# Optimization experiments

Hardware: AMD Instinct MI355X
Metric: run time of the kernel (lower is better)

The kernel has to match this reference:

```python
import jax, jax.numpy as jnp
import numpy as np

B = 262144
IN, H = 2, 50


def setup_inputs() -> dict:
    key = jax.random.key(0)
    ks = jax.random.split(key, 12)
    k = 1.0 / np.sqrt(H)
    u = lambda kk, shape: jax.random.uniform(kk, shape, jnp.float32, -k, k)
    return {
        "s": jax.random.normal(ks[0], (B, IN), jnp.float32),
        "h": jax.random.normal(ks[1], (B, H), jnp.float32),
        "w_ih": u(ks[2], (3 * H, IN)),
        "w_hh": u(ks[3], (3 * H, H)),
        "b_ih": u(ks[4], (3 * H,)),
        "b_hh": u(ks[5], (3 * H,)),
        "actor_w": u(ks[6], (2, H)),
        "actor_b": u(ks[7], (2,)),
        "critic_w": u(ks[8], (1, H)),
        "critic_b": u(ks[9], (1,)),
    }


def reference(s, h, w_ih, w_hh, b_ih, b_hh, actor_w, actor_b, critic_w, critic_b):
    # PyTorch GRUCell gate math (gate order: reset, update, new)
    gi = s @ w_ih.T + b_ih          # [B, 3H]
    gh = h @ w_hh.T + b_hh          # [B, 3H]
    i_r, i_z, i_n = jnp.split(gi, 3, axis=1)
    h_r, h_z, h_n = jnp.split(gh, 3, axis=1)
    r = jax.nn.sigmoid(i_r + h_r)
    z = jax.nn.sigmoid(i_z + h_z)
    n = jnp.tanh(i_n + r * h_n)
    h_new = (1.0 - z) * n + z * h   # [B, H]
    c = h_new @ critic_w.T + critic_b            # [B, 1]
    pi = jax.nn.softmax(h_new @ actor_w.T + actor_b, axis=1)  # [B, 2]
    return h_new, c, pi
```

## Files before the change

### kernel.cpp

```cpp
#include <hip/hip_runtime.h>
#include <hip/hip_bf16.h>


#define BDIM 1024

typedef __bf16 bf16x8 __attribute__((ext_vector_type(8)));
typedef float f32x4 __attribute__((ext_vector_type(4)));
typedef unsigned __attribute__((may_alias)) u32a;
typedef unsigned short __attribute__((may_alias)) u16a;

__device__ __forceinline__ float bf2f(unsigned short u) {
    union { unsigned u; float f; } x; x.u = ((unsigned)u) << 16; return x.f;
}
__device__ __forceinline__ unsigned short f2bf(float f) {
    union { float f; unsigned u; } x; x.f = f;
    unsigned r = x.u + 0x7fffu + ((x.u >> 16) & 1u);
    return (unsigned short)(r >> 16);
}
__device__ __forceinline__ unsigned packbf(float a, float b) {
    union { __hip_bfloat162 h; unsigned u; } c;
    c.h = __float22bfloat162_rn(make_float2(a, b));
    return c.u;
}
__device__ __forceinline__ bf16x8 ldsfrag(const unsigned short* p) {
    bf16x8 v; __builtin_memcpy(&v, p, 16); return v;
}

template <int CTRL>
__device__ __forceinline__ float dpp_add(float v) {
    int s = __builtin_bit_cast(int, v);
    int r = __builtin_amdgcn_update_dpp(s, s, CTRL, 0xf, 0xf, false);
    return v + __builtin_bit_cast(float, r);
}
__device__ __forceinline__ float row16_sum(float v) {
    v = dpp_add<0x128>(v);
    v = dpp_add<0x124>(v);
    v = dpp_add<0x122>(v);
    v = dpp_add<0x121>(v);
    return v;
}

#define PROCESS_TILE(BT, PF)                                                 \
  do {                                                                       \
    const int rowbase = (BT) * 256;                                          \
    asm volatile("" ::: "memory");                                           \
    _Pragma("unroll")                                                        \
    for (int j = 0; j < 6; ++j) {                                            \
        int d = lane + j * 64;                                               \
        int r = d / 25, dk = d - r * 25;                                     \
        xlds32[(R + r) * 36 + dk] = packbf(PF[j].x, PF[j].y);                \
    }                                                                        \
    if (lane < 16)                                                           \
        xlds32[(R + 15) * 36 + 9 + lane] = packbf(PF[6].x, PF[6].y);         \
    else if (lane < 32)                                                      \
        xlds32[(R + lane - 16) * 36 + 25] = packbf(PF[6].x, PF[6].y);        \
    asm volatile("" ::: "memory");                                           \
    float2 srow[4];                                                          \
    _Pragma("unroll")                                                        \
    for (int reg = 0; reg < 4; ++reg)                                        \
        srow[reg] = s2[rowbase + R + quad * 4 + reg];                        \
    const unsigned short* arow = &xlds[(R + c16) * 72 + quad * 8];           \
    bf16x8 a0 = ldsfrag(arow);                                 \
    bf16x8 a1 = ldsfrag(arow + 32);                            \
    float* ob = out + (long long)rowbase * 50;      \
    float hn_r[4][4];                                                        \
    _Pragma("unroll")                                                        \
    for (int t = 0; t < 4; ++t) {                                            \
        f32x4 ar = {0.f,0.f,0.f,0.f}, az = ar, an = ar;                      \
        const int tb = (t * 128 + lane) * 8;   \
        bf16x8 br0 = ldsfrag(&wlds[tb]);                                     \
        bf16x8 br1 = ldsfrag(&wlds[tb + 512]);                               \
        bf16x8 bz0 = ldsfrag(&wlds[tb + 4096]);                              \
        bf16x8 bz1 = ldsfrag(&wlds[tb + 4608]);                              \
        bf16x8 bn0 = ldsfrag(&wlds[tb + 8192]);                              \
        bf16x8 bn1 = ldsfrag(&wlds[tb + 8704]);                              \
        ar = __builtin_amdgcn_mfma_f32_16x16x32_bf16(a0, br0, ar, 0, 0, 0);  \
        ar = __builtin_amdgcn_mfma_f32_16x16x32_bf16(a1, br1, ar, 0, 0, 0);  \
        az = __builtin_amdgcn_mfma_f32_16x16x32_bf16(a0, bz0, az, 0, 0, 0);  \
        az = __builtin_amdgcn_mfma_f32_16x16x32_bf16(a1, bz1, az, 0, 0, 0);  \
        an = __builtin_amdgcn_mfma_f32_16x16x32_bf16(a0, bn0, an, 0, 0, 0);  \
        an = __builtin_amdgcn_mfma_f32_16x16x32_bf16(a1, bn1, an, 0, 0, 0);  \
        int j = t * 16 + c16;                                                \
        _Pragma("unroll")                                                    \
        for (int reg = 0; reg < 4; ++reg) {                                  \
            int lr = R + quad * 4 + reg;          \
            float inn = fmaf(srow[reg].y, wi1[t],                            \
                        fmaf(srow[reg].x, wi0[t], bi[t]));                   \
            float rg = __builtin_amdgcn_rcpf(1.f + __expf(-ar[reg]));        \
            float zg = __builtin_amdgcn_rcpf(1.f + __expf(-az[reg]));        \
            float x = inn + rg * an[reg];                                    \
            float e2 = __expf(2.f * x);    \
            float ng = 1.f - 2.f * __builtin_amdgcn_rcpf(e2 + 1.f);          \
            float hv = bf2f(((const u16a*)xlds)[lr * 72 + j]);               \
            float hnew = fmaf(zg, hv - ng, ng);                              \
            hn_r[reg][t] = (j < 50) ? hnew : 0.f;                            \
            if (j < 50) ob[lr * 50 + j] = hnew;                              \
        }                                                                    \
    }                                                                        \
    float sum0[4], sum1[4], sumc[4];                                         \
    _Pragma("unroll")                                                        \
    for (int reg = 0; reg < 4; ++reg) {                                      \
        float p0 = 0.f, p1 = 0.f, pc = 0.f;                                  \
        _Pragma("unroll")                                                    \
        for (int t = 0; t < 4; ++t) {                                        \
            p0 = fmaf(hn_r[reg][t], aw0[t], p0);                             \
            p1 = fmaf(hn_r[reg][t], aw1[t], p1);                             \
            pc = fmaf(hn_r[reg][t], awc[t], pc);                             \
        }                                                                    \
        sum0[reg] = row16_sum(p0);                                           \
        sum1[reg] = row16_sum(p1);                                           \
        sumc[reg] = row16_sum(pc);                                           \
    }                                                                        \
    if (c16 < 4) {                  \
        float A0 = (c16 == 0) ? sum0[0] : (c16 == 1) ? sum0[1]               \
                 : (c16 == 2) ? sum0[2] : sum0[3];                           \
        float A1 = (c16 == 0) ? sum1[0] : (c16 == 1) ? sum1[1]               \
                 : (c16 == 2) ? sum1[2] : sum1[3];                           \
        float C  = (c16 == 0) ? sumc[0] : (c16 == 1) ? sumc[1]               \
                 : (c16 == 2) ? sumc[2] : sumc[3];                           \
        int gr = rowbase + R + quad * 4 + c16;                               \
        oc[gr] = C + cb;                                                     \
        A0 += ab0; A1 += ab1;                                                \
        float m = fmaxf(A0, A1);                                             \
        float e0 = __expf(A0 - m), e1 = __expf(A1 - m);                      \
        float inv = 1.f / (e0 + e1);                                         \
        float2 pv; pv.x = e0 * inv; pv.y = e1 * inv;                         \
        opi[gr] = pv;                                                        \
    }                                                                        \
  } while (0)

__global__ __launch_bounds__(BDIM, 4) void gru_fused(
    const float* __restrict__ s,
    const float* __restrict__ h,
    const float* __restrict__ w_ih,
    const float* __restrict__ w_hh,
    const float* __restrict__ b_ih,
    const float* __restrict__ b_hh,
    const float* __restrict__ actor_w,
    const float* __restrict__ actor_b,
    const float* __restrict__ critic_w,
    const float* __restrict__ critic_b,
    float* __restrict__ out,
    int Btot, int nTiles)
{
    __shared__ __align__(16) unsigned short xlds[256 * 72];
    __shared__ __align__(16) unsigned short wlds[1536 * 8];

    const int tid  = threadIdx.x;
    const int wave = tid >> 6;
    const int lane = tid & 63;
    const int c16  = lane & 15;
    const int quad = lane >> 4;
    const int R    = wave * 16;

    u32a* xlds32 = (u32a*)xlds;
    const float2* h2 = (const float2*)h;
    const float2* s2 = (const float2*)s;

    const int bt0 = blockIdx.x;
    const int bt1 = bt0 + (int)gridDim.x;
    const bool has2 = (bt1 < nTiles);
    float2 pf0[7], pf1[7];
    {
        long long hb = (long long)(bt0 * 256 + R) * 25;
        #pragma unroll
        for (int j = 0; j < 6; ++j) pf0[j] = h2[hb + lane + j * 64];
        if (lane < 16)      pf0[6] = h2[hb + 384 + lane];
        else if (lane < 32) pf0[6] = s2[bt0 * 256 + R + lane - 16];
    }
    {
        const int pb = has2 ? bt1 : bt0;
        long long hb = (long long)(pb * 256 + R) * 25;
        #pragma unroll
        for (int j = 0; j < 6; ++j) pf1[j] = h2[hb + lane + j * 64];
        if (lane < 16)      pf1[6] = h2[hb + 384 + lane];
        else if (lane < 32) pf1[6] = s2[pb * 256 + R + lane - 16];
    }

    for (int i = tid; i < 256 * 36; i += BDIM)
        xlds32[i] = ((i % 36) == 26) ? 0x00003f80u : 0u;

    for (int e = tid; e < 1536; e += BDIM) {
        int ln = e & 63;
        int ks = (e >> 6) & 1;
        int t  = (e >> 7) & 3;
        int g  = e >> 9;
        int n  = t * 16 + (ln & 15);
        int kbase = ks * 32 + (ln >> 4) * 8;
        unsigned short vals[8];
        if (n < 50) {
            int r = g * 50 + n;
            #pragma unroll
            for (int i = 0; i < 8; ++i) {
                int k = kbase + i;
                float v = 0.f;
                if (k < 50)       v = w_hh[r * 50 + k];
                else if (k == 50) v = (g < 2) ? w_ih[r * 2 + 0] : 0.f;
                else if (k == 51) v = (g < 2) ? w_ih[r * 2 + 1] : 0.f;
                else if (k == 52) {
                    v = b_hh[r];
                    if (g < 2) v += b_ih[r];
                }
                vals[i] = f2bf(v);
            }
        } else {
            #pragma unroll
            for (int i = 0; i < 8; ++i) vals[i] = 0;
        }
        #pragma unroll
        for (int i = 0; i < 8; ++i) wlds[e * 8 + i] = vals[i];
    }

    float wi0[4], wi1[4], bi[4], aw0[4], aw1[4], awc[4];
    #pragma unroll
    for (int t = 0; t < 4; ++t) {
        int j = t * 16 + c16;
        bool ok = (j < 50);
        wi0[t] = ok ? w_ih[(100 + j) * 2 + 0] : 0.f;
        wi1[t] = ok ? w_ih[(100 + j) * 2 + 1] : 0.f;
        bi[t]  = ok ? b_ih[100 + j]           : 0.f;
        aw0[t] = ok ? actor_w[j]              : 0.f;
        aw1[t] = ok ? actor_w[50 + j]         : 0.f;
        awc[t] = ok ? critic_w[j]             : 0.f;
    }
    const float ab0 = actor_b[0], ab1 = actor_b[1], cb = critic_b[0];

    __syncthreads();

    float* oc = out + (long long)Btot * 50;
    float2* opi = (float2*)(out + (long long)Btot * 51);

    PROCESS_TILE(bt0, pf0);
    if (has2) PROCESS_TILE(bt1, pf1);
}

extern "C" void kernel_launch(void* const* d_in, const int* in_sizes, int n_in,
                              void* d_out, int out_size, void* d_ws, size_t ws_size,
                              hipStream_t stream) {
    const float* s        = (const float*)d_in[0];
    const float* h        = (const float*)d_in[1];
    const float* w_ih     = (const float*)d_in[2];
    const float* w_hh     = (const float*)d_in[3];
    const float* b_ih     = (const float*)d_in[4];
    const float* b_hh     = (const float*)d_in[5];
    const float* actor_w  = (const float*)d_in[6];
    const float* actor_b  = (const float*)d_in[7];
    const float* critic_w = (const float*)d_in[8];
    const float* critic_b = (const float*)d_in[9];
    float* out = (float*)d_out;

    int Btot = in_sizes[1] / 50;
    int nTiles = Btot / 256;
    int grid = (nTiles + 1) / 2;

    gru_fused<<<grid, BDIM, 0, stream>>>(s, h, w_ih, w_hh, b_ih, b_hh,
                                         actor_w, actor_b, critic_w, critic_b,
                                         out, Btot, nTiles);
}
```

Before: 144.6 us.

## Prepack GRU weights in a separate kernel and shrink blocks to 512 threads

Result: faster. 140.9 us (-2.6%).

```diff
diff --git a/kernel.cpp b/kernel.cpp
--- a/kernel.cpp
+++ b/kernel.cpp
@@ -2,10 +2,11 @@
 #include <hip/hip_bf16.h>
 
 
-#define BDIM 1024
+#define BDIM 512
 
 typedef __bf16 bf16x8 __attribute__((ext_vector_type(8)));
 typedef float f32x4 __attribute__((ext_vector_type(4)));
+typedef unsigned u32x4 __attribute__((ext_vector_type(4)));
 typedef unsigned __attribute__((may_alias)) u32a;
 typedef unsigned short __attribute__((may_alias)) u16a;
 
@@ -40,10 +41,49 @@
     return v;
 }
 
-#define PROCESS_TILE(BT, PF)                                                 \
+__global__ __launch_bounds__(256, 1) void pack_w(
+    const float* __restrict__ w_ih, const float* __restrict__ w_hh,
+    const float* __restrict__ b_ih, const float* __restrict__ b_hh,
+    u32x4* __restrict__ ws)
+{
+    int e = blockIdx.x * 256 + threadIdx.x;
+    if (e >= 1536) return;
+    int ln = e & 63;
+    int ks = (e >> 6) & 1;
+    int t  = (e >> 7) & 3;
+    int g  = e >> 9;
+    int n  = t * 16 + (ln & 15);
+    int kbase = ks * 32 + (ln >> 4) * 8;
+    unsigned short vals[8];
+    if (n < 50) {
+        int r = g * 50 + n;
+        #pragma unroll
+        for (int i = 0; i < 8; ++i) {
+            int k = kbase + i;
+            float v = 0.f;
+            if (k < 50)       v = w_hh[r * 50 + k];
+            else if (k == 50) v = (g < 2) ? w_ih[r * 2 + 0] : 0.f;
+            else if (k == 51) v = (g < 2) ? w_ih[r * 2 + 1] : 0.f;
+            else if (k == 52) {
+                v = b_hh[r];
+                if (g < 2) v += b_ih[r];
+            }
+            vals[i] = f2bf(v);
+        }
+    } else {
+        #pragma unroll
+        for (int i = 0; i < 8; ++i) vals[i] = 0;
+    }
+    u32x4 o;
+    #pragma unroll
+    for (int i = 0; i < 4; ++i)
+        o[i] = (unsigned)vals[2 * i] | ((unsigned)vals[2 * i + 1] << 16);
+    ws[e] = o;
+}
+
+#define PROCESS_TILE(ROWBASE, PF)                                            \
   do {                                                                       \
-    const int rowbase = (BT) * 256;                                          \
-    asm volatile("" ::: "memory");                                           \
+    const int rowbase = (ROWBASE);                                           \
     _Pragma("unroll")                                                        \
     for (int j = 0; j < 6; ++j) {                                            \
         int d = lane + j * 64;                                               \
@@ -89,7 +129,7 @@
             float rg = __builtin_amdgcn_rcpf(1.f + __expf(-ar[reg]));        \
             float zg = __builtin_amdgcn_rcpf(1.f + __expf(-az[reg]));        \
             float x = inn + rg * an[reg];                                    \
-            float e2 = __expf(2.f * x);    \
+            float e2 = __expf(2.f * x);            \
             float ng = 1.f - 2.f * __builtin_amdgcn_rcpf(e2 + 1.f);          \
             float hv = bf2f(((const u16a*)xlds)[lr * 72 + j]);               \
             float hnew = fmaf(zg, hv - ng, ng);                              \
@@ -133,17 +173,16 @@
     const float* __restrict__ s,
     const float* __restrict__ h,
     const float* __restrict__ w_ih,
-    const float* __restrict__ w_hh,
-    const float* __restrict__ b_ih,
-    const float* __restrict__ b_hh,
     const float* __restrict__ actor_w,
     const float* __restrict__ actor_b,
     const float* __restrict__ critic_w,
     const float* __restrict__ critic_b,
+    const float* __restrict__ b_ih,
+    const u32x4* __restrict__ ws,
     float* __restrict__ out,
     int Btot, int nTiles)
 {
-    __shared__ __align__(16) unsigned short xlds[256 * 72];
+    __shared__ __align__(16) unsigned short xlds[128 * 72];
     __shared__ __align__(16) unsigned short wlds[1536 * 8];
 
     const int tid  = threadIdx.x;
@@ -154,61 +193,35 @@
     const int R    = wave * 16;
 
     u32a* xlds32 = (u32a*)xlds;
+
+    const int rowbase0 = blockIdx.x * 256;
+    const int rowbase1 = rowbase0 + 128;
     const float2* h2 = (const float2*)h;
     const float2* s2 = (const float2*)s;
 
-    const int bt0 = blockIdx.x;
-    const int bt1 = bt0 + (int)gridDim.x;
-    const bool has2 = (bt1 < nTiles);
     float2 pf0[7], pf1[7];
     {
-        long long hb = (long long)(bt0 * 256 + R) * 25;
+        long long hb = (long long)(rowbase0 + R) * 25;
         #pragma unroll
         for (int j = 0; j < 6; ++j) pf0[j] = h2[hb + lane + j * 64];
         if (lane < 16)      pf0[6] = h2[hb + 384 + lane];
-        else if (lane < 32) pf0[6] = s2[bt0 * 256 + R + lane - 16];
+        else if (lane < 32) pf0[6] = s2[rowbase0 + R + lane - 16];
     }
     {
-        const int pb = has2 ? bt1 : bt0;
-        long long hb = (long long)(pb * 256 + R) * 25;
+        long long hb = (long long)(rowbase1 + R) * 25;
         #pragma unroll
         for (int j = 0; j < 6; ++j) pf1[j] = h2[hb + lane + j * 64];
         if (lane < 16)      pf1[6] = h2[hb + 384 + lane];
-        else if (lane < 32) pf1[6] = s2[pb * 256 + R + lane - 16];
-    }
-
-    for (int i = tid; i < 256 * 36; i += BDIM)
-        xlds32[i] = ((i % 36) == 26) ? 0x00003f80u : 0u;
-
-    for (int e = tid; e < 1536; e += BDIM) {
-        int ln = e & 63;
-        int ks = (e >> 6) & 1;
-        int t  = (e >> 7) & 3;
-        int g  = e >> 9;
-        int n  = t * 16 + (ln & 15);
-        int kbase = ks * 32 + (ln >> 4) * 8;
-        unsigned short vals[8];
-        if (n < 50) {
-            int r = g * 50 + n;
-            #pragma unroll
-            for (int i = 0; i < 8; ++i) {
-                int k = kbase + i;
-                float v = 0.f;
-                if (k < 50)       v = w_hh[r * 50 + k];
-                else if (k == 50) v = (g < 2) ? w_ih[r * 2 + 0] : 0.f;
-                else if (k == 51) v = (g < 2) ? w_ih[r * 2 + 1] : 0.f;
-                else if (k == 52) {
-                    v = b_hh[r];
-                    if (g < 2) v += b_ih[r];
-                }
-                vals[i] = f2bf(v);
-            }
-        } else {
-            #pragma unroll
-            for (int i = 0; i < 8; ++i) vals[i] = 0;
-        }
-        #pragma unroll
-        for (int i = 0; i < 8; ++i) wlds[e * 8 + i] = vals[i];
+        else if (lane < 32) pf1[6] = s2[rowbase1 + R + lane - 16];
+    }
+
+    u32x4* wlds16 = (u32x4*)wlds;
+    for (int i = tid; i < 1536; i += BDIM)
+        wlds16[i] = ws[i];
+
+    for (int i = lane; i < 160; i += 64) {
+        int row = R + i / 10, dk = 26 + i % 10;
+        xlds32[row * 36 + dk] = (i % 10 == 0) ? 0x00003f80u : 0u;
     }
 
     float wi0[4], wi1[4], bi[4], aw0[4], aw1[4], awc[4];
@@ -225,13 +238,20 @@
     }
     const float ab0 = actor_b[0], ab1 = actor_b[1], cb = critic_b[0];
 
+    #pragma unroll
+    for (int j = 0; j < 7; ++j) {
+        asm volatile("" :: "v"(pf0[j].x), "v"(pf0[j].y));
+        asm volatile("" :: "v"(pf1[j].x), "v"(pf1[j].y));
+    }
+
     __syncthreads();
 
     float* oc = out + (long long)Btot * 50;
     float2* opi = (float2*)(out + (long long)Btot * 51);
 
-    PROCESS_TILE(bt0, pf0);
-    if (has2) PROCESS_TILE(bt1, pf1);
+    PROCESS_TILE(rowbase0, pf0);
+    asm volatile("" ::: "memory");
+    PROCESS_TILE(rowbase1, pf1);
 }
 
 extern "C" void kernel_launch(void* const* d_in, const int* in_sizes, int n_in,
@@ -250,10 +270,13 @@
     float* out = (float*)d_out;
 
     int Btot = in_sizes[1] / 50;
-    int nTiles = Btot / 256;
-    int grid = (nTiles + 1) / 2;
-
-    gru_fused<<<grid, BDIM, 0, stream>>>(s, h, w_ih, w_hh, b_ih, b_hh,
-                                         actor_w, actor_b, critic_w, critic_b,
-                                         out, Btot, nTiles);
-}
+    int nBlocks = Btot / 256;
+
+    u32x4* ws = (u32x4*)d_ws;
+
+    pack_w<<<6, 256, 0, stream>>>(w_ih, w_hh, b_ih, b_hh, ws);
+    gru_fused<<<nBlocks, BDIM, 0, stream>>>(s, h, w_ih, actor_w, actor_b,
+                                            critic_w, critic_b, b_ih,
+                                            (const u32x4*)ws, out, Btot,
+                                            nBlocks * 2);
+}
```
